# Kernel tuning notes

Measured on AMD Instinct MI355X. Metric: run time of the kernel, lower is better.

Reference implementation:

```python
import jax, jax.numpy as jnp
import numpy as np

VOCAB, EMBED, HIDDEN, NCLS = 50257, 1024, 4096, 3
B, S = 4096, 128


def ternary_quant(w):
    # Per-tensor ternary quantization: scale = mean |w|, weights in {-s, 0, +s}.
    s = jnp.mean(jnp.abs(w))
    return jnp.round(jnp.clip(w / s, -1.0, 1.0)) * s


def layer_norm(x, g, b, eps=1e-5):
    mu = jnp.mean(x, axis=-1, keepdims=True)
    var = jnp.mean(jnp.square(x - mu), axis=-1, keepdims=True)
    return (x - mu) * jax.lax.rsqrt(var + eps) * g + b


def setup_inputs() -> dict:
    key = jax.random.key(0)
    ks = jax.random.split(key, 12)
    input_ids = jax.random.randint(ks[0], (B, S), 0, VOCAB, dtype=jnp.int32)
    emb = jax.random.normal(ks[1], (VOCAB, EMBED), dtype=jnp.float32) * 0.02
    emb = emb.at[0].set(0.0)  # padding_idx=0
    w1 = jax.random.normal(ks[2], (HIDDEN, EMBED), dtype=jnp.float32) * 0.02
    b1 = jnp.zeros((HIDDEN,), jnp.float32)
    w2 = jax.random.normal(ks[3], (HIDDEN // 2, HIDDEN), dtype=jnp.float32) * 0.02
    b2 = jnp.zeros((HIDDEN // 2,), jnp.float32)
    w3 = jax.random.normal(ks[4], (NCLS, HIDDEN // 2), dtype=jnp.float32) * 0.02
    b3 = jnp.zeros((NCLS,), jnp.float32)
    g1 = jnp.ones((HIDDEN,), jnp.float32)
    beta1 = jnp.zeros((HIDDEN,), jnp.float32)
    g2 = jnp.ones((HIDDEN // 2,), jnp.float32)
    beta2 = jnp.zeros((HIDDEN // 2,), jnp.float32)
    return dict(input_ids=input_ids, emb=emb, w1=w1, b1=b1, w2=w2, b2=b2,
                w3=w3, b3=b3, g1=g1, beta1=beta1, g2=g2, beta2=beta2)


def reference(input_ids, emb, w1, b1, w2, b2, w3, b3, g1, beta1, g2, beta2):
    x = emb[input_ids]                                   # (B, S, E)
    mask = (input_ids != 0).astype(x.dtype)[..., None]   # (B, S, 1)
    x = jnp.sum(x * mask, axis=1) / jnp.clip(jnp.sum(mask, axis=1), 1.0)  # (B, E)
    h = jax.nn.gelu(layer_norm(x @ ternary_quant(w1).T + b1, g1, beta1), approximate=False)
    h = jax.nn.gelu(layer_norm(h @ ternary_quant(w2).T + b2, g2, beta2), approximate=False)
    logits = h @ ternary_quant(w3).T + b3                # (B, 3)
    return logits
```

## Files before the change

### kernel.cpp

```cpp
#include <hip/hip_runtime.h>
#include <cstdint>
#include <cstddef>


#define GAS __attribute__((address_space(1)))
#define LAS __attribute__((address_space(3)))

typedef __bf16 bf16x8 __attribute__((ext_vector_type(8)));
typedef float  f32x4  __attribute__((ext_vector_type(4)));
typedef unsigned short u16x8 __attribute__((ext_vector_type(8)));

__device__ __forceinline__ unsigned short f2bf(float f) {
    unsigned int u = __float_as_uint(f);
    u += 0x7FFFu + ((u >> 16) & 1u);
    return (unsigned short)(u >> 16);
}
__device__ __forceinline__ float bf2f(unsigned short h) {
    return __uint_as_float(((unsigned int)h) << 16);
}

static constexpr int BB = 4096;
static constexpr int SS = 128;
static constexpr int EE = 1024;
static constexpr int HH = 4096;
static constexpr int H2D = 2048;
static constexpr int VOCAB = 50257;

static constexpr size_t MiB      = 1024 * 1024;
static constexpr size_t OFF_S    = 0;
static constexpr size_t OFF_X    = 65536;
static constexpr size_t OFF_EMBH = OFF_X + (size_t)BB * EE * 2;
static constexpr size_t SZ_EMBH  = (size_t)VOCAB * EE * 2;
static constexpr size_t OFF_Q1   = OFF_EMBH;
static constexpr size_t OFF_Q2   = OFF_EMBH + 8 * MiB;
static constexpr size_t OFF_C1   = OFF_EMBH + 24 * MiB;
static constexpr size_t OFF_C2   = OFF_EMBH + 24 * MiB;
static constexpr size_t OFF_H2   = OFF_EMBH;
static constexpr size_t OFF_H1   = OFF_EMBH + SZ_EMBH;


__global__ __launch_bounds__(256) void prep2_kernel(const float* __restrict__ e,
                                                    unsigned short* __restrict__ o,
                                                    const float* __restrict__ w1,
                                                    const float* __restrict__ w2,
                                                    double* __restrict__ part1,
                                                    double* __restrict__ part2) {
    const int bid = blockIdx.x;
    const int tid = threadIdx.x;
    const int n8 = (VOCAB * EE) / 8;
    for (int i = bid * 256 + tid; i < n8; i += 2048 * 256) {
        const float4 v0 = ((const float4*)e)[2 * i];
        const float4 v1 = ((const float4*)e)[2 * i + 1];
        union { unsigned short u[8]; uint4 q; } r;
        r.u[0] = f2bf(v0.x); r.u[1] = f2bf(v0.y); r.u[2] = f2bf(v0.z); r.u[3] = f2bf(v0.w);
        r.u[4] = f2bf(v1.x); r.u[5] = f2bf(v1.y); r.u[6] = f2bf(v1.z); r.u[7] = f2bf(v1.w);
        ((uint4*)o)[i] = r.q;
    }
    const int lane = tid & 63, wid = tid >> 6;
    double a1 = 0.0, a2 = 0.0;
    const int n41 = HH * EE / 4;
    for (int i = bid * 256 + tid; i < n41; i += 2048 * 256) {
        const float4 v = ((const float4*)w1)[i];
        a1 += (double)fabsf(v.x) + (double)fabsf(v.y) + (double)fabsf(v.z) + (double)fabsf(v.w);
    }
    const int n42 = H2D * HH / 4;
    for (int i = bid * 256 + tid; i < n42; i += 2048 * 256) {
        const float4 v = ((const float4*)w2)[i];
        a2 += (double)fabsf(v.x) + (double)fabsf(v.y) + (double)fabsf(v.z) + (double)fabsf(v.w);
    }
    for (int off = 32; off; off >>= 1) { a1 += __shfl_down(a1, off); a2 += __shfl_down(a2, off); }
    __shared__ double r1[4], r2[4];
    if (lane == 0) { r1[wid] = a1; r2[wid] = a2; }
    __syncthreads();
    if (tid == 0) {
        part1[bid] = r1[0] + r1[1] + r1[2] + r1[3];
        part2[bid] = r2[0] + r2[1] + r2[2] + r2[3];
    }
}

__global__ __launch_bounds__(256) void reduce_sums(const double* __restrict__ part1,
                                                   const double* __restrict__ part2,
                                                   const float* __restrict__ w3,
                                                   double* __restrict__ sums) {
    const int bid = blockIdx.x, tid = threadIdx.x;
    const int lane = tid & 63, wid = tid >> 6;
    double acc = 0.0;
    if (bid == 0) {
        for (int i = tid; i < 2048; i += 256) acc += part1[i];
    } else if (bid == 1) {
        for (int i = tid; i < 2048; i += 256) acc += part2[i];
    } else {
        for (int i = tid; i < 3 * H2D; i += 256) acc += (double)fabsf(w3[i]);
    }
    for (int o = 32; o; o >>= 1) acc += __shfl_down(acc, o);
    __shared__ double r[4];
    if (lane == 0) r[wid] = acc;
    __syncthreads();
    if (tid == 0) sums[bid] = r[0] + r[1] + r[2] + r[3];
}

__global__ __launch_bounds__(256) void quant_all(const float* __restrict__ w1,
                                                 const float* __restrict__ w2,
                                                 const double* __restrict__ sums,
                                                 unsigned short* __restrict__ q1,
                                                 unsigned short* __restrict__ q2) {
    const int bid = blockIdx.x;
    const float* w; int n8; unsigned short* q; int b0; int nb; double ssum; double dn;
    if (bid < 2048) { w = w1; n8 = HH * EE / 8;  q = q1; b0 = bid;        nb = 2048; ssum = sums[0]; dn = (double)HH * EE;  }
    else            { w = w2; n8 = H2D * HH / 8; q = q2; b0 = bid - 2048; nb = 4096; ssum = sums[1]; dn = (double)H2D * HH; }
    const float inv_s = (float)(dn / ssum);
    for (int i = b0 * 256 + threadIdx.x; i < n8; i += nb * 256) {
        const float4 v0 = ((const float4*)w)[2 * i];
        const float4 v1 = ((const float4*)w)[2 * i + 1];
        union { unsigned short u[8]; uint4 p; } r;
        const float a[8] = {v0.x, v0.y, v0.z, v0.w, v1.x, v1.y, v1.z, v1.w};
        #pragma unroll
        for (int j = 0; j < 8; ++j)
            r.u[j] = f2bf(rintf(fminf(1.f, fmaxf(-1.f, a[j] * inv_s))));
        ((uint4*)q)[i] = r.p;
    }
}

__global__ __launch_bounds__(256) void pool_kernel(const int* __restrict__ ids,
                                                   const unsigned short* __restrict__ embh,
                                                   unsigned short* __restrict__ X) {
    const int tid = threadIdx.x;
    const int row = tid >> 7;
    const int t   = tid & 127;
    __shared__ int sid[256];
    __shared__ int sorted_ids[2][128];
    __shared__ int cnt[2][64];
    __shared__ int pos[2][64];
    __shared__ int nz[2];
    sid[tid] = ids[(size_t)blockIdx.x * 256 + tid];
    if (tid < 128) ((int*)cnt)[tid] = 0;
    if (tid < 2) nz[tid] = 0;
    __syncthreads();
    const int myid = sid[tid];
    const int ph = myid >> 10;
    atomicAdd(&cnt[row][ph], 1);
    if (myid != 0) atomicAdd(&nz[row], 1);
    __syncthreads();
    if (tid < 2) {
        int s = 0;
        #pragma unroll
        for (int p = 0; p < 64; ++p) { pos[tid][p] = s; s += cnt[tid][p]; }
    }
    __syncthreads();
    const int where = atomicAdd(&pos[row][ph], 1);
    sorted_ids[row][where] = myid;
    __syncthreads();

    const int col = t * 8;
    float a[8] = {};
    #pragma unroll 8
    for (int s = 0; s < 128; ++s) {
        const int id = sorted_ids[row][s];
        const u16x8 v = *(const u16x8*)(embh + (size_t)id * EE + col);
        #pragma unroll
        for (int j = 0; j < 8; ++j) a[j] += bf2f(v[j]);
    }
    const int c = nz[row];
    const float inv = 1.f / (float)(c ? c : 1);
    u16x8 ov;
    #pragma unroll
    for (int j = 0; j < 8; ++j) ov[j] = f2bf(a[j] * inv);
    const int b = blockIdx.x * 2 + row;
    *(u16x8*)(X + (size_t)b * EE + col) = ov;
}

#define GEMM_BODY(K_START, K_END)                                                            \
    __shared__ unsigned short sA[128 * 32];                                                  \
    __shared__ unsigned short sB[128 * 32];                                                  \
    const int tid  = threadIdx.x;                                                            \
    const int wid  = tid >> 6;                                                               \
    const int lane = tid & 63;                                                               \
    const int wm = wid >> 1, wn = wid & 1;                                                   \
    const int quad = lane >> 4;                                                              \
    const int l16  = lane & 15;                                                              \
    const int mBase = blockIdx.y * 128;                                                      \
    const int nBase = blockIdx.x * 128;                                                      \
    f32x4 acc[4][4] = {};                                                                    \
    const int srow = tid >> 2;                                                               \
    const int scol = (tid & 3) * 8;                                                          \
    const size_t aOff0 = (size_t)(mBase + srow) * K + scol;                                  \
    const size_t aOff1 = aOff0 + (size_t)64 * K;                                             \
    const size_t bOff0 = (size_t)(nBase + srow) * K + scol;                                  \
    const size_t bOff1 = bOff0 + (size_t)64 * K;                                             \
    unsigned short* ldsA0 = &sA[wid * 512];                                                  \
    unsigned short* ldsA1 = &sA[2048 + wid * 512];                                           \
    unsigned short* ldsB0 = &sB[wid * 512];                                                  \
    unsigned short* ldsB1 = &sB[2048 + wid * 512];                                           \
    for (int k0 = (K_START); k0 < (K_END); k0 += 32) {                                       \
        __syncthreads();                                                                     \
        __builtin_amdgcn_global_load_lds((const GAS void*)(A + aOff0 + k0), (LAS void*)ldsA0, 16, 0, 0); \
        __builtin_amdgcn_global_load_lds((const GAS void*)(A + aOff1 + k0), (LAS void*)ldsA1, 16, 0, 0); \
        __builtin_amdgcn_global_load_lds((const GAS void*)(B + bOff0 + k0), (LAS void*)ldsB0, 16, 0, 0); \
        __builtin_amdgcn_global_load_lds((const GAS void*)(B + bOff1 + k0), (LAS void*)ldsB1, 16, 0, 0); \
        __syncthreads();                                                                     \
        bf16x8 af[4], bfr[4];                                                                \
        _Pragma("unroll")                                                                    \
        for (int i = 0; i < 4; ++i) {                                                        \
            const int rowA = wm * 64 + i * 16 + l16;                                         \
            af[i]  = *(const bf16x8*)(&sA[rowA * 32 + quad * 8]);                            \
            const int rowB = wn * 64 + i * 16 + l16;                                         \
            bfr[i] = *(const bf16x8*)(&sB[rowB * 32 + quad * 8]);                            \
        }                                                                                    \
        _Pragma("unroll")                                                                    \
        for (int i = 0; i < 4; ++i)                                                          \
            _Pragma("unroll")                                                                \
            for (int j = 0; j < 4; ++j)                                                      \
                acc[i][j] = __builtin_amdgcn_mfma_f32_16x16x32_bf16(af[i], bfr[j], acc[i][j], 0, 0, 0); \
    }

__global__ __launch_bounds__(256) void gemm_bt_c16(const unsigned short* __restrict__ A,
                                                   const unsigned short* __restrict__ B,
                                                   unsigned short* __restrict__ C,
                                                   int M, int N, int K) {
    GEMM_BODY(0, K)
    #pragma unroll
    for (int i = 0; i < 4; ++i) {
        const int row0 = mBase + wm * 64 + i * 16 + quad * 4;
        #pragma unroll
        for (int j = 0; j < 4; ++j) {
            const int col = nBase + wn * 64 + j * 16 + l16;
            #pragma unroll
            for (int r = 0; r < 4; ++r)
                C[(size_t)(row0 + r) * N + col] = f2bf(acc[i][j][r]);
        }
    }
}

__global__ __launch_bounds__(256) void gemm_bt_sk2(const unsigned short* __restrict__ A,
                                                   const unsigned short* __restrict__ B,
                                                   float* __restrict__ Cp,
                                                   int M, int N, int K) {
    const int kHalf = K >> 1;
    const int kStart = blockIdx.z * kHalf;
    float* C = Cp + (size_t)blockIdx.z * M * N;
    GEMM_BODY(kStart, kStart + kHalf)
    #pragma unroll
    for (int i = 0; i < 4; ++i) {
        const int row0 = mBase + wm * 64 + i * 16 + quad * 4;
        #pragma unroll
        for (int j = 0; j < 4; ++j) {
            const int col = nBase + wn * 64 + j * 16 + l16;
            #pragma unroll
            for (int r = 0; r < 4; ++r)
                C[(size_t)(row0 + r) * N + col] = acc[i][j][r];
        }
    }
}

__global__ __launch_bounds__(256) void ln_gelu_c16(const unsigned short* __restrict__ Cm,
                                                   const double* __restrict__ ssum, double nw,
                                                   const float* __restrict__ bias,
                                                   const float* __restrict__ gamma,
                                                   const float* __restrict__ beta,
                                                   unsigned short* __restrict__ H, int N) {
    __shared__ float buf[4096];
    __shared__ float redS[4], redQ[4];
    const int row = blockIdx.x, tid = threadIdx.x;
    const int lane = tid & 63, wid = tid >> 6;
    const float s = (float)(ssum[0] / nw);
    float ps = 0.f, pq = 0.f;
    for (int c = tid; c < N; c += 256) {
        const float y = bf2f(Cm[(size_t)row * N + c]) * s + bias[c];
        buf[c] = y;
        ps += y; pq += y * y;
    }
    for (int o = 32; o; o >>= 1) { ps += __shfl_down(ps, o); pq += __shfl_down(pq, o); }
    if (lane == 0) { redS[wid] = ps; redQ[wid] = pq; }
    __syncthreads();
    const float sum = redS[0] + redS[1] + redS[2] + redS[3];
    const float sq  = redQ[0] + redQ[1] + redQ[2] + redQ[3];
    const float mu  = sum / (float)N;
    float var = sq / (float)N - mu * mu;
    var = fmaxf(var, 0.f);
    const float inv = rsqrtf(var + 1e-5f);
    for (int c = tid; c < N; c += 256) {
        const float y = (buf[c] - mu) * inv * gamma[c] + beta[c];
        const float g = 0.5f * y * (1.f + erff(y * 0.70710678118654752f));
        H[(size_t)row * N + c] = f2bf(g);
    }
}

__global__ __launch_bounds__(256) void ln_gelu_2buf(const float* __restrict__ Ca,
                                                    const float* __restrict__ Cb,
                                                    const double* __restrict__ ssum, double nw,
                                                    const float* __restrict__ bias,
                                                    const float* __restrict__ gamma,
                                                    const float* __restrict__ beta,
                                                    unsigned short* __restrict__ H, int N) {
    __shared__ float buf[2048];
    __shared__ float redS[4], redQ[4];
    const int row = blockIdx.x, tid = threadIdx.x;
    const int lane = tid & 63, wid = tid >> 6;
    const float s = (float)(ssum[0] / nw);
    float ps = 0.f, pq = 0.f;
    for (int c = tid; c < N; c += 256) {
        const size_t idx = (size_t)row * N + c;
        const float y = (Ca[idx] + Cb[idx]) * s + bias[c];
        buf[c] = y;
        ps += y; pq += y * y;
    }
    for (int o = 32; o; o >>= 1) { ps += __shfl_down(ps, o); pq += __shfl_down(pq, o); }
    if (lane == 0) { redS[wid] = ps; redQ[wid] = pq; }
    __syncthreads();
    const float sum = redS[0] + redS[1] + redS[2] + redS[3];
    const float sq  = redQ[0] + redQ[1] + redQ[2] + redQ[3];
    const float mu  = sum / (float)N;
    float var = sq / (float)N - mu * mu;
    var = fmaxf(var, 0.f);
    const float inv = rsqrtf(var + 1e-5f);
    for (int c = tid; c < N; c += 256) {
        const float y = (buf[c] - mu) * inv * gamma[c] + beta[c];
        const float g = 0.5f * y * (1.f + erff(y * 0.70710678118654752f));
        H[(size_t)row * N + c] = f2bf(g);
    }
}

__global__ __launch_bounds__(256) void final_kernel(const unsigned short* __restrict__ H2,
                                                    const float* __restrict__ w3,
                                                    const double* __restrict__ ssum,
                                                    const float* __restrict__ b3,
                                                    float* __restrict__ out) {
    const int row = blockIdx.x, tid = threadIdx.x;
    const int lane = tid & 63, wid = tid >> 6;
    const float inv_s3 = (float)((double)(3 * H2D) / ssum[0]);
    float a0 = 0.f, a1 = 0.f, a2 = 0.f;
    for (int k = tid; k < H2D; k += 256) {
        const float h = bf2f(H2[(size_t)row * H2D + k]);
        const float q0 = rintf(fminf(1.f, fmaxf(-1.f, w3[k] * inv_s3)));
        const float q1 = rintf(fminf(1.f, fmaxf(-1.f, w3[H2D + k] * inv_s3)));
        const float q2 = rintf(fminf(1.f, fmaxf(-1.f, w3[2 * H2D + k] * inv_s3)));
        a0 += h * q0; a1 += h * q1; a2 += h * q2;
    }
    for (int o = 32; o; o >>= 1) {
        a0 += __shfl_down(a0, o); a1 += __shfl_down(a1, o); a2 += __shfl_down(a2, o);
    }
    __shared__ float r[3][4];
    if (lane == 0) { r[0][wid] = a0; r[1][wid] = a1; r[2][wid] = a2; }
    __syncthreads();
    if (tid < 3) {
        const float s3 = (float)(ssum[0] / (double)(3 * H2D));
        out[(size_t)row * 3 + tid] =
            (r[tid][0] + r[tid][1] + r[tid][2] + r[tid][3]) * s3 + b3[tid];
    }
}


extern "C" void kernel_launch(void* const* d_in, const int* in_sizes, int n_in,
                              void* d_out, int out_size, void* d_ws, size_t ws_size,
                              hipStream_t stream) {
    const int*   ids = (const int*)d_in[0];
    const float* emb = (const float*)d_in[1];
    const float* w1  = (const float*)d_in[2];
    const float* b1  = (const float*)d_in[3];
    const float* w2  = (const float*)d_in[4];
    const float* b2  = (const float*)d_in[5];
    const float* w3  = (const float*)d_in[6];
    const float* b3  = (const float*)d_in[7];
    const float* g1  = (const float*)d_in[8];
    const float* be1 = (const float*)d_in[9];
    const float* g2  = (const float*)d_in[10];
    const float* be2 = (const float*)d_in[11];
    float* out = (float*)d_out;
    char* ws = (char*)d_ws;

    double*         sums  = (double*)(ws + OFF_S);
    double*         part1 = sums + 8;
    double*         part2 = part1 + 2048;
    unsigned short* X     = (unsigned short*)(ws + OFF_X);
    unsigned short* embh  = (unsigned short*)(ws + OFF_EMBH);
    unsigned short* q1    = (unsigned short*)(ws + OFF_Q1);
    unsigned short* q2    = (unsigned short*)(ws + OFF_Q2);
    unsigned short* C1    = (unsigned short*)(ws + OFF_C1);
    float*          Cp    = (float*)(ws + OFF_C2);
    unsigned short* H1    = (unsigned short*)(ws + OFF_H1);
    unsigned short* H2    = (unsigned short*)(ws + OFF_H2);

    prep2_kernel<<<2048, 256, 0, stream>>>(emb, embh, w1, w2, part1, part2);
    reduce_sums<<<3, 256, 0, stream>>>(part1, part2, w3, sums);
    pool_kernel<<<BB / 2, 256, 0, stream>>>(ids, embh, X);

    quant_all<<<6144, 256, 0, stream>>>(w1, w2, sums, q1, q2);

    gemm_bt_c16<<<dim3(HH / 128, BB / 128), 256, 0, stream>>>(X, q1, C1, BB, HH, EE);
    ln_gelu_c16<<<BB, 256, 0, stream>>>(C1, sums + 0, (double)HH * (double)EE,
                                        b1, g1, be1, H1, HH);
    gemm_bt_sk2<<<dim3(H2D / 128, BB / 128, 2), 256, 0, stream>>>(H1, q2, Cp, BB, H2D, HH);
    ln_gelu_2buf<<<BB, 256, 0, stream>>>(Cp, Cp + (size_t)BB * H2D, sums + 1,
                                         (double)H2D * (double)HH, b2, g2, be2, H2, H2D);
    final_kernel<<<BB, 256, 0, stream>>>(H2, w3, sums + 2, b3, out);
}
```

Baseline: 710.6 us.

## Replace 128x128 GEMMs with pipelined 256x256 double-buffered MFMA kernel

Replaces the simple 128x128 tile GEMM, which synchronises twice per 32-wide k-step, with a 512-thread 256x256 tile kernel. It uses 128KB of dynamic LDS as a double buffer, swizzles LDS addresses to avoid bank conflicts, and interleaves global_load_lds prefetch of the next k-tiles with MFMA groups under explicit waitcnt, barriers and setprio. The goal is to hide global-memory latency and raise arithmetic intensity for both the layer-1 and split-K layer-2 GEMMs. In exchange, the intricate hand-scheduled synchronisation is fragile, and the large LDS footprint limits how many blocks fit per CU.

```diff
diff --git a/kernel.cpp b/kernel.cpp
--- a/kernel.cpp
+++ b/kernel.cpp
@@ -169,58 +169,106 @@
     *(u16x8*)(X + (size_t)b * EE + col) = ov;
 }
 
-#define GEMM_BODY(K_START, K_END)                                                            \
-    __shared__ unsigned short sA[128 * 32];                                                  \
-    __shared__ unsigned short sB[128 * 32];                                                  \
-    const int tid  = threadIdx.x;                                                            \
-    const int wid  = tid >> 6;                                                               \
-    const int lane = tid & 63;                                                               \
-    const int wm = wid >> 1, wn = wid & 1;                                                   \
-    const int quad = lane >> 4;                                                              \
-    const int l16  = lane & 15;                                                              \
-    const int mBase = blockIdx.y * 128;                                                      \
-    const int nBase = blockIdx.x * 128;                                                      \
-    f32x4 acc[4][4] = {};                                                                    \
-    const int srow = tid >> 2;                                                               \
-    const int scol = (tid & 3) * 8;                                                          \
-    const size_t aOff0 = (size_t)(mBase + srow) * K + scol;                                  \
-    const size_t aOff1 = aOff0 + (size_t)64 * K;                                             \
-    const size_t bOff0 = (size_t)(nBase + srow) * K + scol;                                  \
-    const size_t bOff1 = bOff0 + (size_t)64 * K;                                             \
-    unsigned short* ldsA0 = &sA[wid * 512];                                                  \
-    unsigned short* ldsA1 = &sA[2048 + wid * 512];                                           \
-    unsigned short* ldsB0 = &sB[wid * 512];                                                  \
-    unsigned short* ldsB1 = &sB[2048 + wid * 512];                                           \
-    for (int k0 = (K_START); k0 < (K_END); k0 += 32) {                                       \
-        __syncthreads();                                                                     \
-        __builtin_amdgcn_global_load_lds((const GAS void*)(A + aOff0 + k0), (LAS void*)ldsA0, 16, 0, 0); \
-        __builtin_amdgcn_global_load_lds((const GAS void*)(A + aOff1 + k0), (LAS void*)ldsA1, 16, 0, 0); \
-        __builtin_amdgcn_global_load_lds((const GAS void*)(B + bOff0 + k0), (LAS void*)ldsB0, 16, 0, 0); \
-        __builtin_amdgcn_global_load_lds((const GAS void*)(B + bOff1 + k0), (LAS void*)ldsB1, 16, 0, 0); \
-        __syncthreads();                                                                     \
-        bf16x8 af[4], bfr[4];                                                                \
-        _Pragma("unroll")                                                                    \
-        for (int i = 0; i < 4; ++i) {                                                        \
-            const int rowA = wm * 64 + i * 16 + l16;                                         \
-            af[i]  = *(const bf16x8*)(&sA[rowA * 32 + quad * 8]);                            \
-            const int rowB = wn * 64 + i * 16 + l16;                                         \
-            bfr[i] = *(const bf16x8*)(&sB[rowB * 32 + quad * 8]);                            \
-        }                                                                                    \
-        _Pragma("unroll")                                                                    \
-        for (int i = 0; i < 4; ++i)                                                          \
-            _Pragma("unroll")                                                                \
-            for (int j = 0; j < 4; ++j)                                                      \
-                acc[i][j] = __builtin_amdgcn_mfma_f32_16x16x32_bf16(af[i], bfr[j], acc[i][j], 0, 0, 0); \
-    }
-
-__global__ __launch_bounds__(256) void gemm_bt_c16(const unsigned short* __restrict__ A,
-                                                   const unsigned short* __restrict__ B,
-                                                   unsigned short* __restrict__ C,
-                                                   int M, int N, int K) {
-    GEMM_BODY(0, K)
+
+#define FENCE_ asm volatile("" ::: "memory")
+#define SBAR_  do { FENCE_; __builtin_amdgcn_s_barrier(); FENCE_; } while (0)
+#define WAITLGKM_ do { asm volatile("s_waitcnt lgkmcnt(0)" ::: "memory"); __builtin_amdgcn_sched_barrier(0); } while (0)
+
+#define LDA_(dst, b, i, ks) dst = *(const LAS bf16x8*)((LAS char*)lds + (b) * 32768 + aBase0 + (ks) * 8192 + (i) * 1024)
+#define LDB_(dst, b, j, ks) dst = *(const LAS bf16x8*)((LAS char*)lds + (b) * 32768 + bBase0 + (ks) * 8192 + (j) * 1024)
+
+#define STAGE_(gptr, rowBase, t_, slotOff)                                                         \
+    {                                                                                              \
+        const unsigned short* g0_ = (gptr) + (size_t)((rowBase) + srow) * K + kStart + (t_) * 64 + scol; \
+        __builtin_amdgcn_global_load_lds((const GAS void*)g0_,                                     \
+            (LAS void*)((LAS char*)lds + (slotOff) + wid * 1024), 16, 0, 0);                       \
+        __builtin_amdgcn_global_load_lds((const GAS void*)(g0_ + 32),                              \
+            (LAS void*)((LAS char*)lds + (slotOff) + 8192 + wid * 1024), 16, 0, 0);                \
+    }
+
+#define MFMA16_(ib, bfA, jb)                                                                       \
+    _Pragma("unroll") for (int ii = 0; ii < 4; ++ii) {                                             \
+        _Pragma("unroll") for (int jj = 0; jj < 2; ++jj) {                                         \
+            f32x4 c_ = acc[(ib) * 4 + ii][(jb) + jj];                                              \
+            c_ = __builtin_amdgcn_mfma_f32_16x16x32_bf16(af[ii][0], bfA[jj][0], c_, 0, 0, 0);      \
+            c_ = __builtin_amdgcn_mfma_f32_16x16x32_bf16(af[ii][1], bfA[jj][1], c_, 0, 0, 0);      \
+            acc[(ib) * 4 + ii][(jb) + jj] = c_;                                                    \
+        }                                                                                          \
+    }
+
+#define GROUP_(b, t_)                                                                              \
+    {                                                                                              \
+        _Pragma("unroll") for (int ii = 0; ii < 4; ++ii) { LDA_(af[ii][0], b, ii, 0); LDA_(af[ii][1], b, ii, 1); } \
+        _Pragma("unroll") for (int jj = 0; jj < 2; ++jj) { LDB_(bf0[jj][0], b, jj, 0); LDB_(bf0[jj][1], b, jj, 1); } \
+        if ((t_) + 1 < NTI) {                                                                      \
+            STAGE_(A, mBase, (t_) + 1, ((b) ^ 1) * 32768);                                         \
+            STAGE_(A, mBase + 128, (t_) + 1, ((b) ^ 1) * 32768 + 16384);                           \
+        }                                                                                          \
+        SBAR_; WAITLGKM_;                                                                          \
+        __builtin_amdgcn_s_setprio(1); MFMA16_(0, bf0, 0); __builtin_amdgcn_s_setprio(0);          \
+        SBAR_;                                                                                     \
+        _Pragma("unroll") for (int jj = 0; jj < 2; ++jj) { LDB_(bf1[jj][0], b, 2 + jj, 0); LDB_(bf1[jj][1], b, 2 + jj, 1); } \
+        if ((t_) + 1 < NTI) { STAGE_(B, nBase + 128, (t_) + 1, 65536 + ((b) ^ 1) * 32768 + 16384); } \
+        SBAR_; WAITLGKM_;                                                                          \
+        __builtin_amdgcn_s_setprio(1); MFMA16_(0, bf1, 2); __builtin_amdgcn_s_setprio(0);          \
+        SBAR_;                                                                                     \
+        _Pragma("unroll") for (int ii = 0; ii < 4; ++ii) { LDA_(af[ii][0], b, 4 + ii, 0); LDA_(af[ii][1], b, 4 + ii, 1); } \
+        if ((t_) + 2 < NTI) { STAGE_(B, nBase, (t_) + 2, 65536 + (b) * 32768); }                   \
+        SBAR_; WAITLGKM_;                                                                          \
+        __builtin_amdgcn_s_setprio(1); MFMA16_(1, bf0, 0); __builtin_amdgcn_s_setprio(0);          \
+        SBAR_;                                                                                     \
+        __builtin_amdgcn_s_setprio(1); MFMA16_(1, bf1, 2); __builtin_amdgcn_s_setprio(0);          \
+        if ((t_) + 2 < NTI) { asm volatile("s_waitcnt vmcnt(2)" ::: "memory"); }                   \
+        else               { asm volatile("s_waitcnt vmcnt(0)" ::: "memory"); }                    \
+        SBAR_;                                                                                     \
+    }
+
+#define GEMM256_CORE(NT_VAL)                                                                       \
+    extern __shared__ char lds[];                                                                  \
+    constexpr int NTI = (NT_VAL);                                                                  \
+    const int tid  = threadIdx.x;                                                                  \
+    const int wid  = tid >> 6;                                                                     \
+    const int lane = tid & 63;                                                                     \
+    const int wm = wid >> 2, wn = wid & 3;                                                         \
+    const int quad = lane >> 4;                                                                    \
+    const int l16  = lane & 15;                                                                    \
+    const int mBase = blockIdx.y * 256;                                                            \
+    const int nBase = blockIdx.x * 256;                                                            \
+    const int kStart = blockIdx.z * NTI * 64;                                                      \
+                    \
+                    \
+    const int dp   = wid * 1024 + lane * 16;                                                       \
+    const int srow = dp >> 6;                                                                      \
+    const int sb   = dp & 63;                                                                      \
+    const int scol = ((((sb >> 5) & 1) ^ ((srow >> 3) & 1)) << 4) + (((sb >> 4) & 1) << 3);        \
+                           \
+    const int qoff = ((quad ^ (((l16 >> 3) & 1) << 1)) << 4);                                      \
+    const int aBase0 = (wm << 14) + (l16 << 6) + qoff;                                             \
+    const int bBase0 = 65536 + ((wn >> 1) << 14) + ((((wn & 1) << 6) + l16) << 6) + qoff;          \
+    f32x4 acc[8][4] = {};                                                                          \
+    bf16x8 af[4][2], bf0[2][2], bf1[2][2];                                                         \
+              \
+    STAGE_(A, mBase, 0, 0);                                                                        \
+    STAGE_(A, mBase + 128, 0, 16384);                                                              \
+    STAGE_(B, nBase, 0, 65536);                                                                    \
+    STAGE_(B, nBase + 128, 0, 65536 + 16384);                                                      \
+    STAGE_(B, nBase, 1, 65536 + 32768);                                                            \
+    asm volatile("s_waitcnt vmcnt(2)" ::: "memory");                                               \
+    SBAR_;                                                                                         \
+    _Pragma("unroll 1")                                                                            \
+    for (int t = 0; t < NTI; t += 2) {                                                             \
+        GROUP_(0, t)                                                                               \
+        GROUP_(1, t + 1)                                                                           \
+    }
+
+__global__ __launch_bounds__(512, 2) void gemm256_c16(const unsigned short* __restrict__ A,
+                                                      const unsigned short* __restrict__ B,
+                                                      unsigned short* __restrict__ C,
+                                                      int M, int N, int K) {
+    GEMM256_CORE(16)
     #pragma unroll
-    for (int i = 0; i < 4; ++i) {
-        const int row0 = mBase + wm * 64 + i * 16 + quad * 4;
+    for (int i = 0; i < 8; ++i) {
+        const int row0 = mBase + wm * 128 + i * 16 + quad * 4;
         #pragma unroll
         for (int j = 0; j < 4; ++j) {
             const int col = nBase + wn * 64 + j * 16 + l16;
@@ -231,17 +279,15 @@
     }
 }
 
-__global__ __launch_bounds__(256) void gemm_bt_sk2(const unsigned short* __restrict__ A,
-                                                   const unsigned short* __restrict__ B,
-                                                   float* __restrict__ Cp,
-                                                   int M, int N, int K) {
-    const int kHalf = K >> 1;
-    const int kStart = blockIdx.z * kHalf;
+__global__ __launch_bounds__(512, 2) void gemm256_sk2(const unsigned short* __restrict__ A,
+                                                      const unsigned short* __restrict__ B,
+                                                      float* __restrict__ Cp,
+                                                      int M, int N, int K) {
+    GEMM256_CORE(32)
     float* C = Cp + (size_t)blockIdx.z * M * N;
-    GEMM_BODY(kStart, kStart + kHalf)
     #pragma unroll
-    for (int i = 0; i < 4; ++i) {
-        const int row0 = mBase + wm * 64 + i * 16 + quad * 4;
+    for (int i = 0; i < 8; ++i) {
+        const int row0 = mBase + wm * 128 + i * 16 + quad * 4;
         #pragma unroll
         for (int j = 0; j < 4; ++j) {
             const int col = nBase + wn * 64 + j * 16 + l16;
@@ -380,16 +426,25 @@
     unsigned short* H1    = (unsigned short*)(ws + OFF_H1);
     unsigned short* H2    = (unsigned short*)(ws + OFF_H2);
 
+    static int gemmAttrDone = 0;
+    if (!gemmAttrDone) {
+        hipFuncSetAttribute((const void*)gemm256_c16,
+                            hipFuncAttributeMaxDynamicSharedMemorySize, 131072);
+        hipFuncSetAttribute((const void*)gemm256_sk2,
+                            hipFuncAttributeMaxDynamicSharedMemorySize, 131072);
+        gemmAttrDone = 1;
+    }
+
     prep2_kernel<<<2048, 256, 0, stream>>>(emb, embh, w1, w2, part1, part2);
     reduce_sums<<<3, 256, 0, stream>>>(part1, part2, w3, sums);
     pool_kernel<<<BB / 2, 256, 0, stream>>>(ids, embh, X);
 
     quant_all<<<6144, 256, 0, stream>>>(w1, w2, sums, q1, q2);
 
-    gemm_bt_c16<<<dim3(HH / 128, BB / 128), 256, 0, stream>>>(X, q1, C1, BB, HH, EE);
+    gemm256_c16<<<dim3(HH / 256, BB / 256), 512, 131072, stream>>>(X, q1, C1, BB, HH, EE);
     ln_gelu_c16<<<BB, 256, 0, stream>>>(C1, sums + 0, (double)HH * (double)EE,
                                         b1, g1, be1, H1, HH);
-    gemm_bt_sk2<<<dim3(H2D / 128, BB / 128, 2), 256, 0, stream>>>(H1, q2, Cp, BB, H2D, HH);
+    gemm256_sk2<<<dim3(H2D / 256, BB / 256, 2), 512, 131072, stream>>>(H1, q2, Cp, BB, H2D, HH);
     ln_gelu_2buf<<<BB, 256, 0, stream>>>(Cp, Cp + (size_t)BB * H2D, sums + 1,
                                          (double)H2D * (double)HH, b2, g2, be2, H2, H2D);
     final_kernel<<<BB, 256, 0, stream>>>(H2, w3, sums + 2, b3, out);
```

Result: faster. 659.1 us (-7.2%).
